# Performance work log

Measured on AMD Instinct MI355X. Metric: run time of the kernel, lower is better.

The kernel has to match this reference:

```python
import jax, jax.numpy as jnp
import numpy as np


def setup_inputs() -> dict:
    key = jax.random.key(0)
    k1, k2 = jax.random.split(key)
    B, C, T = 64, 16, 32768
    y_pred = jax.random.normal(k1, (B, C, T), dtype=jnp.float32)
    y_true = jax.random.normal(k2, (B, C, T), dtype=jnp.float32)
    return {"y_pred": y_pred, "y_true": y_true}


def reference(y_pred, y_true):
    # Original: for i in 1..T, sum |cumsum(pred[:,:,:i]) - cumsum(true[:,:,:i])|, mean over batch.
    # Prefix position t (0-indexed) appears in all outer iterations i >= t+1, i.e. (T - t) times.
    # => total = mean_b sum_{c,t} |cumsum(pred - true)[b,c,t]| * (T - t)
    B, C, T = y_pred.shape
    c = jnp.cumsum(y_pred - y_true, axis=2)          # (B, C, T)
    w = (T - jnp.arange(T)).astype(y_pred.dtype)     # weight T-t for position t
    total = jnp.sum(jnp.abs(c) * w, axis=(1, 2))     # (B,)
    total = jnp.mean(total)
    scaling = 2.0 / (T * C * (T * C + 1))            # apply_scaling_factor=True
    return scaling * total
```

## Files before the change

kernel.cpp:

```cpp
#include <hip/hip_runtime.h>

#define B_BATCH 64
#define C_CH    16
#define T_LEN   32768
#define THREADS 256
#define VEC     4
#define CHUNK   (THREADS * VEC)
#define NCHUNK  (T_LEN / CHUNK)
#define NROWS   (B_BATCH * C_CH)

__global__ __launch_bounds__(THREADS) void wloss_scan_kernel(
    const float* __restrict__ pred,
    const float* __restrict__ tru,
    double* __restrict__ ws_accum)
{
    const int row  = blockIdx.x;
    const int tid  = threadIdx.x;
    const int lane = tid & 63;
    const int wave = tid >> 6;

    const float4* p4 = (const float4*)(pred + (size_t)row * T_LEN);
    const float4* t4 = (const float4*)(tru  + (size_t)row * T_LEN);

    __shared__ float wtot[2][4];

    float  carry = 0.0f;
    double acc   = 0.0;

    for (int ch = 0; ch < NCHUNK; ++ch) {
        const int v4idx = ch * (CHUNK / VEC) + tid;
        float4 p = p4[v4idx];
        float4 t = t4[v4idx];

        float d0 = p.x - t.x;
        float d1 = p.y - t.y;
        float d2 = p.z - t.z;
        float d3 = p.w - t.w;

        float s1 = d0;
        float s2 = s1 + d1;
        float s3 = s2 + d2;
        float s4 = s3 + d3;

        float v = s4;
        #pragma unroll
        for (int off = 1; off < 64; off <<= 1) {
            float u = __shfl_up(v, off, 64);
            if (lane >= off) v += u;
        }

        const int par = ch & 1;
        if (lane == 63) wtot[par][wave] = v;
        __syncthreads();

        float wprefix = 0.0f;
        float total   = 0.0f;
        #pragma unroll
        for (int w = 0; w < 4; ++w) {
            float wt = wtot[par][w];
            if (w < wave) wprefix += wt;
            total += wt;
        }

        const float excl = carry + wprefix + (v - s4);

        const int   e  = ch * CHUNK + tid * VEC;
        const float w0 = (float)(T_LEN - e);

        float c1 = excl + s1;
        float c2 = excl + s2;
        float c3 = excl + s3;
        float c4 = excl + s4;

        float part = fabsf(c1) * w0
                   + fabsf(c2) * (w0 - 1.0f)
                   + fabsf(c3) * (w0 - 2.0f)
                   + fabsf(c4) * (w0 - 3.0f);
        acc += (double)part;

        carry += total;
    }

    #pragma unroll
    for (int off = 32; off > 0; off >>= 1)
        acc += __shfl_down(acc, off, 64);

    __shared__ double dtot[4];
    if (lane == 0) dtot[wave] = acc;
    __syncthreads();

    if (tid == 0) {
        double s = dtot[0] + dtot[1] + dtot[2] + dtot[3];
        atomicAdd(ws_accum, s);
    }
}

__global__ void wloss_finalize_kernel(const double* __restrict__ ws_accum,
                                      float* __restrict__ out)
{
    const double tc      = (double)T_LEN * (double)C_CH;
    const double scaling = 2.0 / (tc * (tc + 1.0));
    out[0] = (float)(ws_accum[0] * scaling / (double)B_BATCH);
}

extern "C" void kernel_launch(void* const* d_in, const int* in_sizes, int n_in,
                              void* d_out, int out_size, void* d_ws, size_t ws_size,
                              hipStream_t stream)
{
    const float* pred = (const float*)d_in[0];
    const float* tru  = (const float*)d_in[1];
    double*      ws   = (double*)d_ws;
    float*       out  = (float*)d_out;

    hipMemsetAsync(ws, 0, sizeof(double), stream);

    wloss_scan_kernel<<<NROWS, THREADS, 0, stream>>>(pred, tru, ws);
    wloss_finalize_kernel<<<1, 1, 0, stream>>>(ws, out);
}
```

Before: 281.3 us.

## Process 16 elements per thread with register prefetch and fuse finalize into scan

Each thread now scans 16 contiguous elements instead of 4, so each row takes 8 group iterations instead of 32. That cuts block-wide barriers and wave shuffle scans per element. The next group's loads are prefetched into registers while the current group is computed, to hide memory latency. The separate finalize kernel is replaced by a last-block-done counter that writes the output from inside the scan kernel, saving one launch. The costs are higher register use and per-thread strided float4 loads rather than fully coalesced lane-contiguous accesses.

```diff
diff --git a/kernel.cpp b/kernel.cpp
--- a/kernel.cpp
+++ b/kernel.cpp
@@ -4,15 +4,20 @@
 #define C_CH    16
 #define T_LEN   32768
 #define THREADS 256
-#define VEC     4
-#define CHUNK   (THREADS * VEC)
-#define NCHUNK  (T_LEN / CHUNK)
+#define WAVES   4
+#define EPT     16
+#define CHUNK   (64 * EPT)
+#define GROUP   (WAVES * CHUNK)
+#define NGROUP  (T_LEN / GROUP)
 #define NROWS   (B_BATCH * C_CH)
 
-__global__ __launch_bounds__(THREADS) void wloss_scan_kernel(
+struct WsLayout { double sum; unsigned int done; unsigned int pad; };
+
+__global__ __launch_bounds__(THREADS) void wloss_kernel(
     const float* __restrict__ pred,
     const float* __restrict__ tru,
-    double* __restrict__ ws_accum)
+    WsLayout* __restrict__ ws,
+    float* __restrict__ out)
 {
     const int row  = blockIdx.x;
     const int tid  = threadIdx.x;
@@ -22,85 +27,97 @@
     const float4* p4 = (const float4*)(pred + (size_t)row * T_LEN);
     const float4* t4 = (const float4*)(tru  + (size_t)row * T_LEN);
 
-    __shared__ float wtot[2][4];
+    __shared__ float wtot[2][WAVES];
+
+    const int tbase4 = wave * (CHUNK / 4) + lane * (EPT / 4);
+
+    float4 pc[4], tc[4], pn[4], tn[4];
+    #pragma unroll
+    for (int k = 0; k < 4; ++k) {
+        pc[k] = p4[tbase4 + k];
+        tc[k] = t4[tbase4 + k];
+    }
 
     float  carry = 0.0f;
     double acc   = 0.0;
 
-    for (int ch = 0; ch < NCHUNK; ++ch) {
-        const int v4idx = ch * (CHUNK / VEC) + tid;
-        float4 p = p4[v4idx];
-        float4 t = t4[v4idx];
+    for (int g = 0; g < NGROUP; ++g) {
+        if (g + 1 < NGROUP) {
+            const int nb = (g + 1) * (GROUP / 4) + tbase4;
+            #pragma unroll
+            for (int k = 0; k < 4; ++k) {
+                pn[k] = p4[nb + k];
+                tn[k] = t4[nb + k];
+            }
+        }
 
-        float d0 = p.x - t.x;
-        float d1 = p.y - t.y;
-        float d2 = p.z - t.z;
-        float d3 = p.w - t.w;
+        float s[EPT];
+        {
+            const float* pf = (const float*)pc;
+            const float* tf = (const float*)tc;
+            float run = 0.0f;
+            #pragma unroll
+            for (int j = 0; j < EPT; ++j) {
+                run += pf[j] - tf[j];
+                s[j] = run;
+            }
+        }
 
-        float s1 = d0;
-        float s2 = s1 + d1;
-        float s3 = s2 + d2;
-        float s4 = s3 + d3;
-
-        float v = s4;
+        float v = s[EPT - 1];
         #pragma unroll
         for (int off = 1; off < 64; off <<= 1) {
             float u = __shfl_up(v, off, 64);
             if (lane >= off) v += u;
         }
 
-        const int par = ch & 1;
+        const int par = g & 1;
         if (lane == 63) wtot[par][wave] = v;
         __syncthreads();
 
-        float wprefix = 0.0f;
-        float total   = 0.0f;
+        float wpre = 0.0f, gtot = 0.0f;
         #pragma unroll
-        for (int w = 0; w < 4; ++w) {
-            float wt = wtot[par][w];
-            if (w < wave) wprefix += wt;
-            total += wt;
+        for (int w = 0; w < WAVES; ++w) {
+            float t = wtot[par][w];
+            if (w < wave) wpre += t;
+            gtot += t;
         }
 
-        const float excl = carry + wprefix + (v - s4);
+        const float excl = carry + wpre + (v - s[EPT - 1]);
 
-        const int   e  = ch * CHUNK + tid * VEC;
-        const float w0 = (float)(T_LEN - e);
-
-        float c1 = excl + s1;
-        float c2 = excl + s2;
-        float c3 = excl + s3;
-        float c4 = excl + s4;
-
-        float part = fabsf(c1) * w0
-                   + fabsf(c2) * (w0 - 1.0f)
-                   + fabsf(c3) * (w0 - 2.0f)
-                   + fabsf(c4) * (w0 - 3.0f);
+        const int   e0 = g * GROUP + wave * CHUNK + lane * EPT;
+        const float w0 = (float)(T_LEN - e0);
+        float part = 0.0f;
+        #pragma unroll
+        for (int j = 0; j < EPT; ++j)
+            part += fabsf(excl + s[j]) * (w0 - (float)j);
         acc += (double)part;
 
-        carry += total;
+        carry += gtot;
+
+        #pragma unroll
+        for (int k = 0; k < 4; ++k) { pc[k] = pn[k]; tc[k] = tn[k]; }
     }
 
     #pragma unroll
     for (int off = 32; off > 0; off >>= 1)
         acc += __shfl_down(acc, off, 64);
 
-    __shared__ double dtot[4];
+    __shared__ double dtot[WAVES];
     if (lane == 0) dtot[wave] = acc;
     __syncthreads();
 
     if (tid == 0) {
-        double s = dtot[0] + dtot[1] + dtot[2] + dtot[3];
-        atomicAdd(ws_accum, s);
+        double sblk = dtot[0] + dtot[1] + dtot[2] + dtot[3];
+        atomicAdd(&ws->sum, sblk);
+        __threadfence();
+        unsigned int prev = atomicAdd(&ws->done, 1u);
+        if (prev == NROWS - 1) {
+            double total = atomicAdd(&ws->sum, 0.0);
+            const double tc_     = (double)T_LEN * (double)C_CH;
+            const double scaling = 2.0 / (tc_ * (tc_ + 1.0));
+            out[0] = (float)(total * scaling / (double)B_BATCH);
+        }
     }
-}
-
-__global__ void wloss_finalize_kernel(const double* __restrict__ ws_accum,
-                                      float* __restrict__ out)
-{
-    const double tc      = (double)T_LEN * (double)C_CH;
-    const double scaling = 2.0 / (tc * (tc + 1.0));
-    out[0] = (float)(ws_accum[0] * scaling / (double)B_BATCH);
 }
 
 extern "C" void kernel_launch(void* const* d_in, const int* in_sizes, int n_in,
@@ -109,11 +126,10 @@
 {
     const float* pred = (const float*)d_in[0];
     const float* tru  = (const float*)d_in[1];
-    double*      ws   = (double*)d_ws;
+    WsLayout*    ws   = (WsLayout*)d_ws;
     float*       out  = (float*)d_out;
 
-    hipMemsetAsync(ws, 0, sizeof(double), stream);
+    hipMemsetAsync(ws, 0, sizeof(WsLayout), stream);
 
-    wloss_scan_kernel<<<NROWS, THREADS, 0, stream>>>(pred, tru, ws);
-    wloss_finalize_kernel<<<1, 1, 0, stream>>>(ws, out);
+    wloss_kernel<<<NROWS, THREADS, 0, stream>>>(pred, tru, ws, out);
 }
```

New measurement: 320.3 us. 13.9% more time.

## Use single-wave blocks with register-prefetched loads and fused finalize

Applied to the files above, without the earlier changes.

Each row is now scanned by one 64-lane wave instead of four waves. This removes the shared-memory wave-total exchange and the per-chunk __syncthreads. Loads are software-pipelined through a 16-deep register ring buffer of float4s so memory latency overlaps with the scan work. The separate finalize kernel is folded into the main kernel through a last-block-done atomic counter. The trade-off is only 1024 small blocks of 64 threads with heavy register use, so there may be too few waves to saturate HBM bandwidth on the GPU.

```diff
diff --git a/kernel.cpp b/kernel.cpp
--- a/kernel.cpp
+++ b/kernel.cpp
@@ -3,104 +3,97 @@
 #define B_BATCH 64
 #define C_CH    16
 #define T_LEN   32768
-#define THREADS 256
-#define VEC     4
-#define CHUNK   (THREADS * VEC)
+#define NROWS   (B_BATCH * C_CH)
+#define WSZ     64
+#define CHUNK   256
 #define NCHUNK  (T_LEN / CHUNK)
-#define NROWS   (B_BATCH * C_CH)
+#define DEPTH   16
 
-__global__ __launch_bounds__(THREADS) void wloss_scan_kernel(
+struct WsLayout { double sum; unsigned int done; unsigned int pad; };
+
+__global__ __launch_bounds__(WSZ, 1) void wloss_kernel(
     const float* __restrict__ pred,
     const float* __restrict__ tru,
-    double* __restrict__ ws_accum)
+    WsLayout* __restrict__ ws,
+    float* __restrict__ out)
 {
     const int row  = blockIdx.x;
-    const int tid  = threadIdx.x;
-    const int lane = tid & 63;
-    const int wave = tid >> 6;
+    const int lane = threadIdx.x;
 
     const float4* p4 = (const float4*)(pred + (size_t)row * T_LEN);
     const float4* t4 = (const float4*)(tru  + (size_t)row * T_LEN);
 
-    __shared__ float wtot[2][4];
+    float4 pb[DEPTH], tb[DEPTH];
+    #pragma unroll
+    for (int k = 0; k < DEPTH; ++k) {
+        pb[k] = p4[k * 64 + lane];
+        tb[k] = t4[k * 64 + lane];
+    }
 
     float  carry = 0.0f;
     double acc   = 0.0;
 
-    for (int ch = 0; ch < NCHUNK; ++ch) {
-        const int v4idx = ch * (CHUNK / VEC) + tid;
-        float4 p = p4[v4idx];
-        float4 t = t4[v4idx];
+    #pragma unroll 1
+    for (int base = 0; base < NCHUNK; base += DEPTH) {
+        #pragma unroll
+        for (int k = 0; k < DEPTH; ++k) {
+            const int c = base + k;
+            float4 p = pb[k];
+            float4 t = tb[k];
 
-        float d0 = p.x - t.x;
-        float d1 = p.y - t.y;
-        float d2 = p.z - t.z;
-        float d3 = p.w - t.w;
+            const int nc = c + DEPTH;
+            if (nc < NCHUNK) {
+                pb[k] = p4[nc * 64 + lane];
+                tb[k] = t4[nc * 64 + lane];
+            }
 
-        float s1 = d0;
-        float s2 = s1 + d1;
-        float s3 = s2 + d2;
-        float s4 = s3 + d3;
+            float d0 = p.x - t.x;
+            float d1 = p.y - t.y;
+            float d2 = p.z - t.z;
+            float d3 = p.w - t.w;
+            float s1 = d0;
+            float s2 = s1 + d1;
+            float s3 = s2 + d2;
+            float s4 = s3 + d3;
 
-        float v = s4;
-        #pragma unroll
-        for (int off = 1; off < 64; off <<= 1) {
-            float u = __shfl_up(v, off, 64);
-            if (lane >= off) v += u;
+            float v = s4;
+            #pragma unroll
+            for (int off = 1; off < 64; off <<= 1) {
+                float u = __shfl_up(v, off, 64);
+                if (lane >= off) v += u;
+            }
+
+            const float excl = carry + (v - s4);
+            const float ctot = __shfl(v, 63, 64);
+
+            const int   e0 = c * CHUNK + lane * 4;
+            const float w0 = (float)(T_LEN - e0);
+
+            float part = fabsf(excl + s1) * w0
+                       + fabsf(excl + s2) * (w0 - 1.0f)
+                       + fabsf(excl + s3) * (w0 - 2.0f)
+                       + fabsf(excl + s4) * (w0 - 3.0f);
+            acc += (double)part;
+
+            carry += ctot;
         }
-
-        const int par = ch & 1;
-        if (lane == 63) wtot[par][wave] = v;
-        __syncthreads();
-
-        float wprefix = 0.0f;
-        float total   = 0.0f;
-        #pragma unroll
-        for (int w = 0; w < 4; ++w) {
-            float wt = wtot[par][w];
-            if (w < wave) wprefix += wt;
-            total += wt;
-        }
-
-        const float excl = carry + wprefix + (v - s4);
-
-        const int   e  = ch * CHUNK + tid * VEC;
-        const float w0 = (float)(T_LEN - e);
-
-        float c1 = excl + s1;
-        float c2 = excl + s2;
-        float c3 = excl + s3;
-        float c4 = excl + s4;
-
-        float part = fabsf(c1) * w0
-                   + fabsf(c2) * (w0 - 1.0f)
-                   + fabsf(c3) * (w0 - 2.0f)
-                   + fabsf(c4) * (w0 - 3.0f);
-        acc += (double)part;
-
-        carry += total;
     }
 
     #pragma unroll
     for (int off = 32; off > 0; off >>= 1)
         acc += __shfl_down(acc, off, 64);
 
-    __shared__ double dtot[4];
-    if (lane == 0) dtot[wave] = acc;
-    __syncthreads();
-
-    if (tid == 0) {
-        double s = dtot[0] + dtot[1] + dtot[2] + dtot[3];
-        atomicAdd(ws_accum, s);
+    if (lane == 0) {
+        atomicAdd(&ws->sum, acc);
+        __threadfence();
+        unsigned int prev = atomicAdd(&ws->done, 1u);
+        if (prev == NROWS - 1) {
+            double total = atomicAdd(&ws->sum, 0.0);
+            const double tc_     = (double)T_LEN * (double)C_CH;
+            const double scaling = 2.0 / (tc_ * (tc_ + 1.0));
+            out[0] = (float)(total * scaling / (double)B_BATCH);
+        }
     }
-}
-
-__global__ void wloss_finalize_kernel(const double* __restrict__ ws_accum,
-                                      float* __restrict__ out)
-{
-    const double tc      = (double)T_LEN * (double)C_CH;
-    const double scaling = 2.0 / (tc * (tc + 1.0));
-    out[0] = (float)(ws_accum[0] * scaling / (double)B_BATCH);
 }
 
 extern "C" void kernel_launch(void* const* d_in, const int* in_sizes, int n_in,
@@ -109,11 +102,10 @@
 {
     const float* pred = (const float*)d_in[0];
     const float* tru  = (const float*)d_in[1];
-    double*      ws   = (double*)d_ws;
+    WsLayout*    ws   = (WsLayout*)d_ws;
     float*       out  = (float*)d_out;
 
-    hipMemsetAsync(ws, 0, sizeof(double), stream);
+    hipMemsetAsync(ws, 0, sizeof(WsLayout), stream);
 
-    wloss_scan_kernel<<<NROWS, THREADS, 0, stream>>>(pred, tru, ws);
-    wloss_finalize_kernel<<<1, 1, 0, stream>>>(ws, out);
+    wloss_kernel<<<NROWS, WSZ, 0, stream>>>(pred, tru, ws, out);
 }
```

After: 312.8 us. +11.2%, slower.
